# Kernel optimization log

Hardware: AMD Instinct MI355X
Metric: run time of the kernel (lower is better)

## Reference

```python
import jax, jax.numpy as jnp
import numpy as np

N_CLASSES = 1000
FEAT_DIM = 256
N = 65536


def setup_inputs() -> dict:
    key = jax.random.key(0)
    k1, k2, k3 = jax.random.split(key, 3)
    gt = jax.random.randint(k1, (N, N_CLASSES), 0, 2, dtype=jnp.int32)
    features = jax.random.normal(k2, (N, FEAT_DIM), dtype=jnp.float32)
    centers = jax.random.normal(k3, (N_CLASSES, FEAT_DIM), dtype=jnp.float32)
    return {"gt": gt, "features": features, "centers": centers}


def reference(gt, features, centers):
    # loss = (1/N) * sum_c sum_{i : gt[i,c] > 0} ||features[i] - centers[c]||^2
    # Vectorized via ||f||^2 + ||c||^2 - 2 f.c  (replaces the per-class python loop)
    mask = (gt > 0).astype(features.dtype)                      # [N, C]
    f_sq = jnp.sum(features * features, axis=1)                 # [N]
    c_sq = jnp.sum(centers * centers, axis=1)                   # [C]
    cross = features @ centers.T                                # [N, C]
    dist = f_sq[:, None] + c_sq[None, :] - 2.0 * cross          # [N, C]
    num_instances = features.shape[0]
    return jnp.sum(mask * dist) / num_instances
```

## Files before the change

kernel.cpp:

```cpp
#include <hip/hip_runtime.h>
#include <stdint.h>

#define N_ROWS 65536
#define N_CLS  1000
#define KPAD   1024
#define FEAT   256
#define MT     64
#define BK     64
#define NIT    (KPAD/BK)

typedef short bf16x8 __attribute__((ext_vector_type(8)));
typedef float f32x4  __attribute__((ext_vector_type(4)));

__device__ __forceinline__ ushort f32_to_bf16_rne(float f) {
    union { float f; uint32_t u; } x; x.f = f;
    uint32_t u = x.u + 0x7FFFu + ((x.u >> 16) & 1u);
    return (ushort)(u >> 16);
}

__global__ __launch_bounds__(256) void prep_kernel(const float* __restrict__ centers,
                                                   ushort* __restrict__ Bfrag,
                                                   float* __restrict__ csq,
                                                   float* __restrict__ out) {
    const int c = blockIdx.x;
    const int n = threadIdx.x;
    float v = 0.f;
    if (c < N_CLS) v = centers[(size_t)c * FEAT + n];

    const int it   = c >> 6;
    const int ks   = (c >> 5) & 1;
    const int quad = (c >> 3) & 3;
    const int j    = c & 7;
    const int w    = n >> 6;
    const int nt   = (n >> 4) & 3;
    const int ml   = n & 15;
    const int lane = quad * 16 + ml;
    const size_t idx = ((size_t)(((it * 2 + ks) * 4 + w) * 4 + nt) * 64 + lane) * 8 + j;
    Bfrag[idx] = f32_to_bf16_rne(v);

    float sq = v * v;
    #pragma unroll
    for (int off = 32; off > 0; off >>= 1) sq += __shfl_down(sq, off);
    __shared__ float red[4];
    if ((threadIdx.x & 63) == 0) red[threadIdx.x >> 6] = sq;
    __syncthreads();
    if (threadIdx.x == 0) {
        csq[c] = red[0] + red[1] + red[2] + red[3];
        if (c == 0) out[0] = 0.f;
    }
}

__global__ __launch_bounds__(256, 3) void main_kernel(const int* __restrict__ gt,
                                                      const float* __restrict__ features,
                                                      const ushort* __restrict__ Bfrag,
                                                      const float* __restrict__ csq,
                                                      float* __restrict__ out) {
    __shared__ ushort As[2 * 2 * 4 * 64 * 8];
    __shared__ float  rcS[256];
    __shared__ float  t2S[256];
    __shared__ float  rowcnt[MT];
    __shared__ float  t2row[MT];
    __shared__ float  blockred[4];

    const int tid  = threadIdx.x;
    const int m0   = blockIdx.x * MT;
    const int r    = tid >> 2;
    const int kc   = tid & 3;
    const int lane = tid & 63;
    const int w    = tid >> 6;
    const int ml   = lane & 15;
    const int quad = lane >> 4;

    f32x4 acc[4][4];
    #pragma unroll
    for (int i = 0; i < 4; i++)
        #pragma unroll
        for (int j = 0; j < 4; j++)
            #pragma unroll
            for (int k = 0; k < 4; k++) acc[i][j][k] = 0.f;

    int   rci = 0;
    float t2  = 0.f;
    const int* gtrow = gt + (size_t)(m0 + r) * N_CLS;

    const int mt_w = r >> 4, ml_w = r & 15;
    const int ks_w = kc >> 1, qb = (kc & 1) * 2;
    const int xw   = (ml_w >> 3) | (ks_w << 1) | ((kc & 1) << 2);
    const int slot0 = (((ks_w * 4 + mt_w) * 64) + (qb * 16 + ml_w)) ^ xw;
    const int slot1 = (((ks_w * 4 + mt_w) * 64) + ((qb + 1) * 16 + ml_w)) ^ xw;
    ushort* const wptr0 = As + slot0 * 8;
    ushort* const wptr1 = As + slot1 * 8;

    const int xr0 = ((lane >> 3) & 1) | (0 << 1) | (((lane >> 5) & 1) << 2);
    const int lx0 = (lane ^ xr0) * 8;
    const int lx1 = (lane ^ (xr0 | 2)) * 8;

    auto load_gt = [&](int it, int (&vv)[16]) {
        const int kb = it * BK + kc * 16;
        if (kb + 16 <= N_CLS) {
            const int4* p = (const int4*)(gtrow + kb);
            int4 a0 = p[0], a1 = p[1], a2 = p[2], a3 = p[3];
            vv[0]=a0.x;  vv[1]=a0.y;  vv[2]=a0.z;  vv[3]=a0.w;
            vv[4]=a1.x;  vv[5]=a1.y;  vv[6]=a1.z;  vv[7]=a1.w;
            vv[8]=a2.x;  vv[9]=a2.y;  vv[10]=a2.z; vv[11]=a2.w;
            vv[12]=a3.x; vv[13]=a3.y; vv[14]=a3.z; vv[15]=a3.w;
        } else {
            #pragma unroll
            for (int j = 0; j < 16; j++) {
                int k = kb + j;
                vv[j] = (k < N_CLS) ? gtrow[k] : 0;
            }
        }
    };

    auto convert_store = [&](int buf, int it, const int (&vv)[16]) {
        const int kb = it * BK + kc * 16;
        const float4* cp = (const float4*)(csq + kb);
        float4 q0 = cp[0], q1 = cp[1], q2 = cp[2], q3 = cp[3];
        float cs[16] = {q0.x,q0.y,q0.z,q0.w, q1.x,q1.y,q1.z,q1.w,
                        q2.x,q2.y,q2.z,q2.w, q3.x,q3.y,q3.z,q3.w};
        uint32_t u[8];
        #pragma unroll
        for (int j = 0; j < 8; j++)
            u[j] = (uint32_t)(vv[2*j] + (vv[2*j+1] << 16)) * 0x3F80u;
        #pragma unroll
        for (int j = 0; j < 16; j++) {
            rci += vv[j];
            t2  += (float)vv[j] * cs[j];
        }
        uint4* d0 = (uint4*)(wptr0 + buf * 4096);
        uint4* d1 = (uint4*)(wptr1 + buf * 4096);
        *d0 = make_uint4(u[0], u[1], u[2], u[3]);
        *d1 = make_uint4(u[4], u[5], u[6], u[7]);
    };

    {
        int v0[16];
        load_gt(0, v0);
        convert_store(0, 0, v0);
    }
    __syncthreads();

    int cur = 0;
    const ushort* bbase = Bfrag + ((size_t)w * 4) * 64 * 8 + (size_t)lane * 8;

    for (int it = 0; it < NIT; ++it) {
        const bool hn = (it + 1 < NIT);

        bf16x8 b0[4], b1[4];
        {
            const ushort* p0 = bbase + (size_t)(it * 2 + 0) * (4 * 4 * 64 * 8);
            const ushort* p1 = bbase + (size_t)(it * 2 + 1) * (4 * 4 * 64 * 8);
            #pragma unroll
            for (int nt = 0; nt < 4; ++nt) b0[nt] = *(const bf16x8*)(p0 + nt * 64 * 8);
            #pragma unroll
            for (int nt = 0; nt < 4; ++nt) b1[nt] = *(const bf16x8*)(p1 + nt * 64 * 8);
        }

        int vn[16];
        if (hn) load_gt(it + 1, vn);

        #pragma unroll
        for (int ks = 0; ks < 2; ++ks) {
            const int lx = ks ? lx1 : lx0;
            bf16x8 af[4];
            #pragma unroll
            for (int mt = 0; mt < 4; mt++)
                af[mt] = *(const bf16x8*)(As + cur * 4096 + (ks * 4 + mt) * 512 + lx);
            #pragma unroll
            for (int mt = 0; mt < 4; mt++)
                #pragma unroll
                for (int nt = 0; nt < 4; nt++)
                    acc[mt][nt] = __builtin_amdgcn_mfma_f32_16x16x32_bf16(
                        af[mt], ks ? b1[nt] : b0[nt], acc[mt][nt], 0, 0, 0);
        }

        if (hn) convert_store(cur ^ 1, it + 1, vn);
        __syncthreads();
        cur ^= 1;
    }

    rcS[tid] = (float)rci;
    t2S[tid] = t2;
    __syncthreads();
    if (tid < MT) {
        rowcnt[tid] = rcS[tid*4] + rcS[tid*4+1] + rcS[tid*4+2] + rcS[tid*4+3];
        t2row[tid]  = t2S[tid*4] + t2S[tid*4+1] + t2S[tid*4+2] + t2S[tid*4+3];
    }
    __syncthreads();

    float part = 0.f;
    #pragma unroll
    for (int mt = 0; mt < 4; mt++) {
        #pragma unroll
        for (int nt = 0; nt < 4; nt++) {
            const int n = w * 64 + nt * 16 + ml;
            #pragma unroll
            for (int reg = 0; reg < 4; reg++) {
                const int ri = mt * 16 + quad * 4 + reg;
                const float f = features[(size_t)(m0 + ri) * FEAT + n];
                const float T = acc[mt][nt][reg];
                part += f * (rowcnt[ri] * f - 2.f * T) + t2row[ri] * (1.f / 256.f);
            }
        }
    }
    #pragma unroll
    for (int off = 32; off > 0; off >>= 1) part += __shfl_down(part, off);
    if (lane == 0) blockred[w] = part;
    __syncthreads();
    if (tid == 0)
        atomicAdd(out, (blockred[0] + blockred[1] + blockred[2] + blockred[3]) *
                           (1.f / (float)N_ROWS));
}

extern "C" void kernel_launch(void* const* d_in, const int* in_sizes, int n_in,
                              void* d_out, int out_size, void* d_ws, size_t ws_size,
                              hipStream_t stream) {
    const int*   gt       = (const int*)d_in[0];
    const float* features = (const float*)d_in[1];
    const float* centers  = (const float*)d_in[2];
    float*       out      = (float*)d_out;

    ushort* Bfrag = (ushort*)d_ws;
    float*  csq   = (float*)((char*)d_ws + (size_t)FEAT * KPAD * 2);

    prep_kernel<<<KPAD, 256, 0, stream>>>(centers, Bfrag, csq, out);
    main_kernel<<<N_ROWS / MT, 256, 0, stream>>>(gt, features, Bfrag, csq, out);
}
```

Before: 423.1 us.

## Deepen gt prefetch to two iterations and stage center norms in LDS

The main loop now keeps two register buffers of gt values, so global loads are issued two iterations ahead of their conversion into the LDS A tile. This gives each load more time to arrive before it is needed, which matters because the kernel streams a large gt matrix from memory. The squared center norms are also copied into shared memory once per block instead of being re-read from global memory on every iteration. The extra register buffer may raise register pressure and could hurt occupancy under launch_bounds(256,3).

```diff
diff --git a/kernel.cpp b/kernel.cpp
--- a/kernel.cpp
+++ b/kernel.cpp
@@ -56,6 +56,7 @@
                                                       const float* __restrict__ csq,
                                                       float* __restrict__ out) {
     __shared__ ushort As[2 * 2 * 4 * 64 * 8];
+    __shared__ float  csqS[KPAD];
     __shared__ float  rcS[256];
     __shared__ float  t2S[256];
     __shared__ float  rowcnt[MT];
@@ -91,7 +92,7 @@
     ushort* const wptr0 = As + slot0 * 8;
     ushort* const wptr1 = As + slot1 * 8;
 
-    const int xr0 = ((lane >> 3) & 1) | (0 << 1) | (((lane >> 5) & 1) << 2);
+    const int xr0 = ((lane >> 3) & 1) | (((lane >> 5) & 1) << 2);
     const int lx0 = (lane ^ xr0) * 8;
     const int lx1 = (lane ^ (xr0 | 2)) * 8;
 
@@ -115,7 +116,7 @@
 
     auto convert_store = [&](int buf, int it, const int (&vv)[16]) {
         const int kb = it * BK + kc * 16;
-        const float4* cp = (const float4*)(csq + kb);
+        const float4* cp = (const float4*)&csqS[kb];
         float4 q0 = cp[0], q1 = cp[1], q2 = cp[2], q3 = cp[3];
         float cs[16] = {q0.x,q0.y,q0.z,q0.w, q1.x,q1.y,q1.z,q1.w,
                         q2.x,q2.y,q2.z,q2.w, q3.x,q3.y,q3.z,q3.w};
@@ -134,39 +135,23 @@
         *d1 = make_uint4(u[4], u[5], u[6], u[7]);
     };
 
-    {
-        int v0[16];
-        load_gt(0, v0);
-        convert_store(0, 0, v0);
-    }
-    __syncthreads();
-
-    int cur = 0;
     const ushort* bbase = Bfrag + ((size_t)w * 4) * 64 * 8 + (size_t)lane * 8;
 
-    for (int it = 0; it < NIT; ++it) {
-        const bool hn = (it + 1 < NIT);
-
+    auto mfma_iter = [&](int buf, int it) {
         bf16x8 b0[4], b1[4];
-        {
-            const ushort* p0 = bbase + (size_t)(it * 2 + 0) * (4 * 4 * 64 * 8);
-            const ushort* p1 = bbase + (size_t)(it * 2 + 1) * (4 * 4 * 64 * 8);
-            #pragma unroll
-            for (int nt = 0; nt < 4; ++nt) b0[nt] = *(const bf16x8*)(p0 + nt * 64 * 8);
-            #pragma unroll
-            for (int nt = 0; nt < 4; ++nt) b1[nt] = *(const bf16x8*)(p1 + nt * 64 * 8);
-        }
-
-        int vn[16];
-        if (hn) load_gt(it + 1, vn);
-
+        const ushort* p0 = bbase + (size_t)(it * 2 + 0) * (4 * 4 * 64 * 8);
+        const ushort* p1 = bbase + (size_t)(it * 2 + 1) * (4 * 4 * 64 * 8);
+        #pragma unroll
+        for (int nt = 0; nt < 4; ++nt) b0[nt] = *(const bf16x8*)(p0 + nt * 64 * 8);
+        #pragma unroll
+        for (int nt = 0; nt < 4; ++nt) b1[nt] = *(const bf16x8*)(p1 + nt * 64 * 8);
         #pragma unroll
         for (int ks = 0; ks < 2; ++ks) {
             const int lx = ks ? lx1 : lx0;
             bf16x8 af[4];
             #pragma unroll
             for (int mt = 0; mt < 4; mt++)
-                af[mt] = *(const bf16x8*)(As + cur * 4096 + (ks * 4 + mt) * 512 + lx);
+                af[mt] = *(const bf16x8*)(As + buf * 4096 + (ks * 4 + mt) * 512 + lx);
             #pragma unroll
             for (int mt = 0; mt < 4; mt++)
                 #pragma unroll
@@ -174,10 +159,28 @@
                     acc[mt][nt] = __builtin_amdgcn_mfma_f32_16x16x32_bf16(
                         af[mt], ks ? b1[nt] : b0[nt], acc[mt][nt], 0, 0, 0);
         }
-
-        if (hn) convert_store(cur ^ 1, it + 1, vn);
-        __syncthreads();
-        cur ^= 1;
+    };
+
+    int gtA[16], gtB[16];
+    {
+        *(float4*)&csqS[tid * 4] = *(const float4*)&csq[tid * 4];
+        load_gt(0, gtA);
+        __syncthreads();
+        convert_store(0, 0, gtA);
+        load_gt(1, gtA);
+        __syncthreads();
+    }
+
+    for (int it = 0; it < NIT; it += 2) {
+        if (it + 2 < NIT) load_gt(it + 2, gtB);
+        mfma_iter(0, it);
+        if (it + 1 < NIT) convert_store(1, it + 1, gtA);
+        __syncthreads();
+
+        if (it + 3 < NIT) load_gt(it + 3, gtA);
+        mfma_iter(1, it + 1);
+        if (it + 2 < NIT) convert_store(0, it + 2, gtB);
+        __syncthreads();
     }
 
     rcS[tid] = (float)rci;
```

Measured after the change: 420.6 us. No clear change (-0.6%).
